# Performance work log

Hardware: AMD Instinct MI355X
Metric: run time of the kernel (lower is better)

## Reference

```python
import jax, jax.numpy as jnp
import numpy as np
from jax import lax

B, C, H, W = 2, 96, 64, 64
D_INNER, D_STATE, DT_RANK, K = 192, 16, 6, 4
EPS = 1e-5


def _ln(x, g, b):
    mu = jnp.mean(x, -1, keepdims=True)
    var = jnp.var(x, -1, keepdims=True)
    return (x - mu) * lax.rsqrt(var + EPS) * g + b


def setup_inputs() -> dict:
    key = jax.random.key(0)
    ks = jax.random.split(key, 10)
    f = lambda k, s, sc=0.02: jax.random.normal(k, s, dtype=jnp.float32) * sc
    return {
        "rgb": jax.random.normal(ks[0], (B, C, H, W), dtype=jnp.float32),
        "t": jax.random.normal(ks[1], (B, C, H, W), dtype=jnp.float32),
        "conv_w": f(ks[2], (C, 2 * C, 3, 3), 0.05),
        "conv_b": jnp.zeros((C,), jnp.float32),
        "bn_gamma": jnp.ones((C,), jnp.float32),
        "bn_beta": jnp.zeros((C,), jnp.float32),
        "bn_mean": jnp.zeros((C,), jnp.float32),
        "bn_var": jnp.ones((C,), jnp.float32),
        "ln_gamma": jnp.ones((C,), jnp.float32),
        "ln_beta": jnp.zeros((C,), jnp.float32),
        "in_proj_w": f(ks[3], (2 * D_INNER, C)),
        "dwconv_w": f(ks[4], (D_INNER, 1, 3, 3), 0.1),
        "dwconv_b": jnp.zeros((D_INNER,), jnp.float32),
        "x_proj_w": f(ks[5], (K, DT_RANK + 2 * D_STATE, D_INNER)),
        "dt_w": f(ks[6], (K, D_INNER, DT_RANK), 0.1),
        "dt_b": jnp.full((K, D_INNER), float(np.log(np.expm1(0.01))), jnp.float32),
        "A_logs": jnp.log(jnp.tile(jnp.arange(1, D_STATE + 1, dtype=jnp.float32), (K * D_INNER, 1))),
        "Ds": jnp.ones((K * D_INNER,), jnp.float32),
        "out_norm_gamma": jnp.ones((D_INNER,), jnp.float32),
        "out_norm_beta": jnp.zeros((D_INNER,), jnp.float32),
        "out_proj_w": f(ks[7], (C, D_INNER)),
    }


def _forward(rgb, t, conv_w, conv_b, bn_gamma, bn_beta, bn_mean, bn_var,
             ln_gamma, ln_beta, in_proj_w, dwconv_w, dwconv_b, x_proj_w,
             dt_w, dt_b, A_logs, Ds, out_norm_gamma, out_norm_beta, out_proj_w):
    dn = ("NCHW", "OIHW", "NCHW")
    # BasicConv: conv + BN(eval) + ReLU (dropout inactive in eval)
    x = jnp.concatenate([rgb, t], axis=1)
    x = lax.conv_general_dilated(x, conv_w, (1, 1), "SAME", dimension_numbers=dn)
    x = x + conv_b[None, :, None, None]
    x = (x - bn_mean[None, :, None, None]) * lax.rsqrt(bn_var[None, :, None, None] + EPS)
    x = x * bn_gamma[None, :, None, None] + bn_beta[None, :, None, None]
    x = jax.nn.relu(x)
    # permute to (B,H,W,C) and LayerNorm over channels
    x = _ln(jnp.transpose(x, (0, 2, 3, 1)), ln_gamma, ln_beta)
    # ---- SS2D ----
    xz = jnp.einsum("bhwc,ec->bhwe", x, in_proj_w)  # e = 2*d_inner
    xc, z = jnp.split(xz, 2, axis=-1)
    xc = jnp.transpose(xc, (0, 3, 1, 2))  # (B, d_inner, H, W)
    xc = lax.conv_general_dilated(xc, dwconv_w, (1, 1), "SAME",
                                  dimension_numbers=dn, feature_group_count=D_INNER)
    xc = jax.nn.silu(xc + dwconv_b[None, :, None, None])
    L = H * W
    # cross-scan: row-major, col-major, and their reverses -> (B,4,d,L)
    x_flat = xc.reshape(B, D_INNER, L)
    x_tr = jnp.transpose(xc, (0, 1, 3, 2)).reshape(B, D_INNER, L)
    xs = jnp.stack([x_flat, x_tr], axis=1)
    xs = jnp.concatenate([xs, xs[..., ::-1]], axis=1)  # (B,K,d,L)
    x_dbl = jnp.einsum("bkdl,kcd->bkcl", xs, x_proj_w)
    dts = x_dbl[:, :, :DT_RANK]
    Bs = x_dbl[:, :, DT_RANK:DT_RANK + D_STATE]  # (B,K,N,L)
    Cs = x_dbl[:, :, DT_RANK + D_STATE:]         # (B,K,N,L)
    dts = jnp.einsum("bkrl,kdr->bkdl", dts, dt_w)
    A = -jnp.exp(A_logs).reshape(K, D_INNER, D_STATE)
    Dsk = Ds.reshape(K, D_INNER)
    delta = jax.nn.softplus(dts + dt_b[None, :, :, None])  # (B,K,d,L)
    du = delta * xs

    def step(h, inp):
        dl, dul, Bl, Cl = inp  # (B,K,d),(B,K,d),(B,K,N),(B,K,N)
        h = h * jnp.exp(dl[..., None] * A) + dul[..., None] * Bl[:, :, None, :]
        y = jnp.einsum("bkdn,bkn->bkd", h, Cl)
        return h, y

    h0 = jnp.zeros((B, K, D_INNER, D_STATE), delta.dtype)
    _, ys = lax.scan(step, h0, (
        jnp.transpose(delta, (3, 0, 1, 2)),
        jnp.transpose(du, (3, 0, 1, 2)),
        jnp.transpose(Bs, (3, 0, 1, 2)),
        jnp.transpose(Cs, (3, 0, 1, 2)),
    ))
    out_y = jnp.transpose(ys, (1, 2, 3, 0)) + xs * Dsk[None, :, :, None]  # (B,K,d,L)
    # merge four scan directions back to row-major order
    inv_y = out_y[:, 2:4, :, ::-1]
    wh_y = jnp.transpose(out_y[:, 1].reshape(B, D_INNER, W, H), (0, 1, 3, 2)).reshape(B, D_INNER, L)
    invwh_y = jnp.transpose(inv_y[:, 1].reshape(B, D_INNER, W, H), (0, 1, 3, 2)).reshape(B, D_INNER, L)
    y = out_y[:, 0] + inv_y[:, 0] + wh_y + invwh_y  # (B,d,L)
    y = jnp.transpose(y, (0, 2, 1)).reshape(B, H, W, D_INNER)
    y = _ln(y, out_norm_gamma, out_norm_beta)
    y = y * jax.nn.silu(z)
    out = jnp.einsum("bhwd,cd->bhwc", y, out_proj_w)
    return jnp.transpose(out, (0, 3, 1, 2))  # (B,C,H,W)


def reference(rgb, t, conv_w, conv_b, bn_gamma, bn_beta, bn_mean, bn_var,
              ln_gamma, ln_beta, in_proj_w, dwconv_w, dwconv_b, x_proj_w,
              dt_w, dt_b, A_logs, Ds, out_norm_gamma, out_norm_beta, out_proj_w):
    return _forward(rgb, t, conv_w, conv_b, bn_gamma, bn_beta, bn_mean, bn_var,
                    ln_gamma, ln_beta, in_proj_w, dwconv_w, dwconv_b, x_proj_w,
                    dt_w, dt_b, A_logs, Ds, out_norm_gamma, out_norm_beta, out_proj_w)
```

## Files before the change

kernel.cpp:

```cpp
#include <hip/hip_runtime.h>
#include <math.h>

#define HW 4096
#define CC 96
#define DD 192
#define NS 16
#define KK 4
#define LC 64
#define NC 64
#define NCH (8*DD*NS)

__device__ __forceinline__ float siluf(float x){ return x / (1.f + __expf(-x)); }
__device__ __forceinline__ float softplus_fast(float x){ return (x > 20.f) ? x : __logf(1.f + __expf(x)); }

__device__ __forceinline__ int lmap_xs(int k, int l){
  if (k == 1) return ((l & 63) << 6) | (l >> 6);
  if (k == 2) return (HW - 1) - l;
  if (k == 3) { int r = (HW - 1) - l; return ((r & 63) << 6) | (r >> 6); }
  return l;
}

__global__ void k_prep(const float* __restrict__ cw, const float* __restrict__ xpw,
                       float* __restrict__ wT, float* __restrict__ xpwT){
  int o = blockIdx.x*256 + threadIdx.x;
  if (o < 165888){
    int co = o % 96; int rest = o / 96; int tap = rest % 9; int cig = rest / 9;
    wT[o] = cw[((size_t)co*192 + cig)*9 + tap];
  } else if (o < 165888 + 29184){
    int o2 = o - 165888;
    int c = o2 % 38; int rest = o2 / 38; int d = rest % 192; int k = rest / 192;
    xpwT[o2] = xpw[((size_t)(k*38 + c))*192 + d];
  }
}

__global__ void __launch_bounds__(256, 4)
k_conv1(const float* __restrict__ rgb, const float* __restrict__ tt,
        const float* __restrict__ wT, float* __restrict__ pbuf){
  __shared__ float in_lds[6][6][68];
  __shared__ __align__(16) float w_lds[6][9][64];
  int bi = blockIdx.x;
  int kc  = bi & 15;        int ci0 = kc*12;
  int cog = (bi >> 4) & 1;  int co0 = cog*48;
  int b   = (bi >> 5) & 1;
  int pt  = bi >> 6;        int h0 = pt*4;
  int tid = threadIdx.x;
  int pg = tid & 31;  int r = pg >> 3;  int w0 = (pg & 7)*8;
  int cg = tid >> 5;  int co_t = cg*6;

  float acc[6][8];
  #pragma unroll
  for (int c = 0; c < 6; ++c)
    #pragma unroll
    for (int p = 0; p < 8; ++p) acc[c][p] = 0.f;

  for (int s = 0; s < 2; ++s){
    if (s) __syncthreads();
    if (tid < 72){ int side = tid & 1; int rr = (tid % 12) >> 1; int ci = tid / 12;
                   in_lds[ci][rr][side ? 65 : 0] = 0.f; }
    for (int i = tid; i < 2304; i += 256){
      int ci = i / 384; int rem = i - ci*384; int rr = rem >> 6; int w = rem & 63;
      int grow = h0 - 1 + rr;
      int cig = ci0 + s*6 + ci;
      float v = 0.f;
      if (grow >= 0 && grow < 64){
        const float* src = (cig < CC) ? (rgb + (size_t)(b*CC+cig)*HW)
                                      : (tt  + (size_t)(b*CC+cig-CC)*HW);
        v = src[grow*64 + w];
      }
      in_lds[ci][rr][w+1] = v;
    }
    for (int i = tid; i < 2592; i += 256){
      int co = i % 48; int rest = i / 48; int tap = rest % 9; int ci = rest / 9;
      w_lds[ci][tap][(co/6)*8 + (co%6)] =
          wT[((size_t)(ci0 + s*6 + ci)*9 + tap)*96 + co0 + co];
    }
    __syncthreads();
    #pragma unroll
    for (int ci = 0; ci < 6; ++ci){
      float rowv[3][10];
      #pragma unroll
      for (int rr = 0; rr < 3; ++rr){
        const float* rp = &in_lds[ci][r+rr][w0];
        float4 a = *(const float4*)rp;
        float4 bb = *(const float4*)(rp+4);
        float2 cc = *(const float2*)(rp+8);
        rowv[rr][0]=a.x; rowv[rr][1]=a.y; rowv[rr][2]=a.z; rowv[rr][3]=a.w;
        rowv[rr][4]=bb.x; rowv[rr][5]=bb.y; rowv[rr][6]=bb.z; rowv[rr][7]=bb.w;
        rowv[rr][8]=cc.x; rowv[rr][9]=cc.y;
      }
      #pragma unroll
      for (int tap = 0; tap < 9; ++tap){
        int rt = tap/3, ct = tap - rt*3;
        float4 wa = *(const float4*)&w_lds[ci][tap][cg*8];
        float2 wb = *(const float2*)&w_lds[ci][tap][cg*8+4];
        float wv[6] = {wa.x, wa.y, wa.z, wa.w, wb.x, wb.y};
        #pragma unroll
        for (int p = 0; p < 8; ++p){
          float iv = rowv[rt][p + ct];
          #pragma unroll
          for (int c = 0; c < 6; ++c) acc[c][p] += wv[c]*iv;
        }
      }
    }
  }
  #pragma unroll
  for (int p = 0; p < 8; ++p){
    int pix = (h0 + r)*64 + w0 + p;
    float* o = pbuf + (((size_t)kc*2 + b)*HW + pix)*CC + co0 + co_t;
    float2 o0 = {acc[0][p], acc[1][p]};
    float2 o1 = {acc[2][p], acc[3][p]};
    float2 o2 = {acc[4][p], acc[5][p]};
    *(float2*)&o[0] = o0; *(float2*)&o[2] = o1; *(float2*)&o[4] = o2;
  }
}

__global__ void k_convred(const float* __restrict__ pbuf, const float* __restrict__ cb,
                          const float* __restrict__ bng, const float* __restrict__ bnb,
                          const float* __restrict__ bnm, const float* __restrict__ bnv,
                          const float* __restrict__ lng, const float* __restrict__ lnb,
                          float* __restrict__ xn){
  __shared__ float sm[4], sm2[4], smu[2], srs[2];
  int tid = threadIdx.x;
  int half = tid >> 7;
  int c = tid & 127;
  int pixg = blockIdx.x*2 + half;
  int b = pixg >> 12; int pix = pixg & (HW-1);
  float v = 0.f;
  if (c < CC){
    #pragma unroll
    for (int kc = 0; kc < 16; ++kc)
      v += pbuf[(((size_t)kc*2 + b)*HW + pix)*CC + c];
    v += cb[c];
    v = (v - bnm[c]) * rsqrtf(bnv[c] + 1e-5f);
    v = v * bng[c] + bnb[c];
    v = fmaxf(v, 0.f);
  }
  float s = v, s2 = v*v;
  #pragma unroll
  for (int off = 32; off; off >>= 1){ s += __shfl_down(s, off); s2 += __shfl_down(s2, off); }
  if ((tid & 63) == 0){ sm[tid>>6] = s; sm2[tid>>6] = s2; }
  __syncthreads();
  if (tid < 2){
    float ts = sm[2*tid] + sm[2*tid+1];
    float ts2 = sm2[2*tid] + sm2[2*tid+1];
    float mu = ts * (1.f/CC);
    float var = ts2 * (1.f/CC) - mu*mu;
    smu[tid] = mu; srs[tid] = rsqrtf(var + 1e-5f);
  }
  __syncthreads();
  if (c < CC)
    xn[(size_t)pixg*CC + c] = (v - smu[half])*srs[half]*lng[c] + lnb[c];
}

__global__ void k_inproj(const float* __restrict__ xn, const float* __restrict__ ipw,
                         float* __restrict__ xz){
  __shared__ float As[64][97];
  __shared__ __align__(16) float Bs[96][68];
  int p0 = blockIdx.x*64;
  int e0 = blockIdx.y*64;
  int tid = threadIdx.x;
  for (int idx = tid; idx < 64*96; idx += 256){
    int r = idx/96, c = idx - r*96;
    As[r][c] = xn[(size_t)(p0+r)*96 + c];
  }
  for (int idx = tid; idx < 96*64; idx += 256){
    int c = idx/64, e = idx - c*64;
    Bs[c][e] = ipw[(size_t)(e0+e)*96 + c];
  }
  __syncthreads();
  int tx = tid & 15, ty = tid >> 4;
  float acc[4][4] = {};
  for (int c = 0; c < 96; ++c){
    float a[4];
    #pragma unroll
    for (int i = 0; i < 4; ++i) a[i] = As[ty*4+i][c];
    float4 bb = *(const float4*)&Bs[c][tx*4];
    float bv[4] = {bb.x, bb.y, bb.z, bb.w};
    #pragma unroll
    for (int i = 0; i < 4; ++i)
      #pragma unroll
      for (int j = 0; j < 4; ++j) acc[i][j] += a[i]*bv[j];
  }
  for (int i = 0; i < 4; ++i){
    float4 o = {acc[i][0], acc[i][1], acc[i][2], acc[i][3]};
    *(float4*)&xz[(size_t)(p0+ty*4+i)*384 + e0 + tx*4] = o;
  }
}

__global__ void k_dwconv(const float* __restrict__ xz, const float* __restrict__ dww,
                         const float* __restrict__ dwb, float* __restrict__ xc){
  int gid = blockIdx.x*256 + threadIdx.x;
  int dq = gid % 48; int bp = gid / 48;
  int d = dq*4;
  int pix = bp & (HW-1); int b = bp >> 12;
  int h = pix >> 6, w = pix & 63;
  float4 acc = *(const float4*)&dwb[d];
  float wreg[4][9];
  #pragma unroll
  for (int j = 0; j < 4; ++j)
    #pragma unroll
    for (int t = 0; t < 9; ++t) wreg[j][t] = dww[(d+j)*9 + t];
  #pragma unroll
  for (int dh = -1; dh <= 1; ++dh){
    int hh = h + dh;
    if (hh < 0 || hh > 63) continue;
    #pragma unroll
    for (int dw2 = -1; dw2 <= 1; ++dw2){
      int ww = w + dw2;
      if (ww < 0 || ww > 63) continue;
      float4 v = *(const float4*)&xz[((size_t)b*HW + hh*64 + ww)*384 + d];
      int t = (dh+1)*3 + (dw2+1);
      acc.x += v.x*wreg[0][t];
      acc.y += v.y*wreg[1][t];
      acc.z += v.z*wreg[2][t];
      acc.w += v.w*wreg[3][t];
    }
  }
  float4 o = {siluf(acc.x), siluf(acc.y), siluf(acc.z), siluf(acc.w)};
  *(float4*)&xc[(size_t)bp*DD + d] = o;
}

__global__ void __launch_bounds__(320)
k_xdbl(const float* __restrict__ xc, const float* __restrict__ xpwT,
       const float* __restrict__ dtw, const float* __restrict__ dtb,
       float* __restrict__ Bsb, float* __restrict__ Csb, float* __restrict__ dlt){
  __shared__ float xs_t[48*20];
  __shared__ float w_t[48*80];
  __shared__ float dts_s[2][16][8];
  int blk = blockIdx.x;
  int lt = blk & 255; int p = (blk >> 8) & 1; int b = blk >> 9;
  int l0 = lt*16;
  int tid = threadIdx.x;
  int lg = tid & 15, cg = tid >> 4;
  int c0 = cg*4;
  int b4kA = b*4 + p, b4kB = b*4 + p + 2;
  int wc = tid % 76;
  int wg = tid / 76;
  int kkW = (wc < 38) ? p : (p + 2);
  int ccW = (wc < 38) ? wc : wc - 38;

  float acc[4] = {0.f, 0.f, 0.f, 0.f};
  for (int ch = 0; ch < 4; ++ch){
    int d0 = ch*48;
    if (ch) __syncthreads();
    if (tid < 192){
      int j = tid & 15; int dq = tid >> 4;
      int l = l0 + j;
      int lm = (p == 0) ? l : (((l & 63) << 6) | (l >> 6));
      float4 v = *(const float4*)&xc[((size_t)b*HW + lm)*DD + d0 + dq*4];
      xs_t[(dq*4+0)*20 + j] = v.x;
      xs_t[(dq*4+1)*20 + j] = v.y;
      xs_t[(dq*4+2)*20 + j] = v.z;
      xs_t[(dq*4+3)*20 + j] = v.w;
    }
    if (wg < 4){
      #pragma unroll
      for (int dd = wg; dd < 48; dd += 4)
        w_t[dd*80 + wc] = xpwT[((size_t)kkW*192 + d0 + dd)*38 + ccW];
    }
    __syncthreads();
    #pragma unroll 4
    for (int dd = 0; dd < 48; ++dd){
      float4 wv = *(const float4*)&w_t[dd*80 + c0];
      float xv = xs_t[dd*20 + lg];
      acc[0] += wv.x*xv;
      acc[1] += wv.y*xv;
      acc[2] += wv.z*xv;
      acc[3] += wv.w*xv;
    }
  }
  {
    int lf = l0 + lg;
    int lr = HW - 1 - lf;
    #pragma unroll
    for (int j = 0; j < 4; ++j){
      int c = c0 + j;
      float v = acc[j];
      if      (c <  6) dts_s[0][lg][c] = v;
      else if (c < 22) Bsb [((size_t)b4kA*HW + lf)*NS + (c-6)]   = v;
      else if (c < 38) Csb [((size_t)b4kA*HW + lf)*NS + (c-22)]  = v;
      else if (c < 44) dts_s[1][lg][c-38] = v;
      else if (c < 60) Bsb [((size_t)b4kB*HW + lr)*NS + (c-44)]  = v;
      else if (c < 76) Csb [((size_t)b4kB*HW + lr)*NS + (c-60)]  = v;
    }
  }
  __syncthreads();

  for (int o = tid; o < 6144; o += 320){
    int dir = (o >= 3072) ? 1 : 0;
    int oo = o - dir*3072;
    int lj = oo / 192;
    int d  = oo - lj*192;
    int k  = dir ? (p + 2) : p;
    int b4k = dir ? b4kB : b4kA;
    int lout = dir ? (HW - 1 - (l0 + lj)) : (l0 + lj);
    const float* t = dts_s[dir][lj];
    const float* wp = &dtw[(size_t)(k*DD + d)*6];
    float s = dtb[k*DD + d] + t[0]*wp[0] + t[1]*wp[1] + t[2]*wp[2]
                            + t[3]*wp[3] + t[4]*wp[4] + t[5]*wp[5];
    dlt[((size_t)b4k*HW + lout)*DD + d] = softplus_fast(s);
  }
}

__global__ void k_scan1(const float* __restrict__ dlt, const float* __restrict__ xc,
                        const float* __restrict__ Bsb, const float* __restrict__ Alog,
                        float* __restrict__ Ac, float* __restrict__ Bc){
  int tid = blockIdx.x*256 + threadIdx.x;
  int ng = tid & 3;
  int t2 = tid >> 2;
  int d = t2 % DD;
  int rest = t2 / DD;
  int chunk = rest & (NC-1);
  int b4k = rest >> 6;
  int k = b4k & 3, b = b4k >> 2;
  float4 Af = *(const float4*)&Alog[(size_t)(k*DD+d)*NS + ng*4];
  float Av[4] = {-__expf(Af.x), -__expf(Af.y), -__expf(Af.z), -__expf(Af.w)};
  float h[4] = {0.f,0.f,0.f,0.f};
  float ap[4] = {1.f,1.f,1.f,1.f};
  int l0 = chunk*LC;
  const float* dp  = dlt + ((size_t)b4k*HW + l0)*DD + d;
  const float4* Bp4 = (const float4*)(Bsb + ((size_t)b4k*HW + l0)*NS) + ng;
  const float* xcb = xc + (size_t)b*HW*DD + d;
  float dvc = dp[0];
  float xvc = xcb[(size_t)lmap_xs(k, l0)*DD];
  float4 Bvc = Bp4[0];
  #pragma unroll 4
  for (int i = 0; i < LC; ++i){
    float dvn = 0.f, xvn = 0.f; float4 Bvn = {0.f,0.f,0.f,0.f};
    if (i+1 < LC){
      dvn = dp[(size_t)(i+1)*DD];
      xvn = xcb[(size_t)lmap_xs(k, l0+i+1)*DD];
      Bvn = Bp4[(size_t)(i+1)*4];
    }
    float du = dvc*xvc;
    float a0 = __expf(dvc*Av[0]), a1 = __expf(dvc*Av[1]),
          a2 = __expf(dvc*Av[2]), a3 = __expf(dvc*Av[3]);
    h[0] = h[0]*a0 + du*Bvc.x; ap[0] *= a0;
    h[1] = h[1]*a1 + du*Bvc.y; ap[1] *= a1;
    h[2] = h[2]*a2 + du*Bvc.z; ap[2] *= a2;
    h[3] = h[3]*a3 + du*Bvc.w; ap[3] *= a3;
    dvc = dvn; xvc = xvn; Bvc = Bvn;
  }
  size_t base = (size_t)chunk*NCH + (size_t)(b4k*DD + d)*NS + ng*4;
  *(float4*)&Ac[base] = make_float4(ap[0],ap[1],ap[2],ap[3]);
  *(float4*)&Bc[base] = make_float4(h[0],h[1],h[2],h[3]);
}

__global__ void k_scan2(float* __restrict__ Ac, const float* __restrict__ Bc){
  int chain = blockIdx.x*256 + threadIdx.x;
  float h = 0.f;
  for (int c = 0; c < NC; ++c){
    size_t idx = (size_t)c*NCH + chain;
    float a = Ac[idx], bv = Bc[idx];
    Ac[idx] = h;
    h = a*h + bv;
  }
}

__global__ void k_scan3(const float* __restrict__ dlt, const float* __restrict__ xc,
                        const float* __restrict__ Bsb, const float* __restrict__ Csb,
                        const float* __restrict__ Alog, const float* __restrict__ hst,
                        float* __restrict__ ys){
  int tid = blockIdx.x*256 + threadIdx.x;
  int ng = tid & 3;
  int t2 = tid >> 2;
  int d = t2 % DD;
  int rest = t2 / DD;
  int chunk = rest & (NC-1);
  int b4k = rest >> 6;
  int k = b4k & 3, b = b4k >> 2;
  float4 Af = *(const float4*)&Alog[(size_t)(k*DD+d)*NS + ng*4];
  float Av[4] = {-__expf(Af.x), -__expf(Af.y), -__expf(Af.z), -__expf(Af.w)};
  size_t hbase = (size_t)chunk*NCH + (size_t)(b4k*DD + d)*NS + ng*4;
  float4 hf = *(const float4*)&hst[hbase];
  float h[4] = {hf.x, hf.y, hf.z, hf.w};
  int l0 = chunk*LC;
  const float* dp  = dlt + ((size_t)b4k*HW + l0)*DD + d;
  const float4* Bp4 = (const float4*)(Bsb + ((size_t)b4k*HW + l0)*NS) + ng;
  const float4* Cp4 = (const float4*)(Csb + ((size_t)b4k*HW + l0)*NS) + ng;
  const float* xcb = xc + (size_t)b*HW*DD + d;
  float* yp = ys + ((size_t)b4k*HW + l0)*DD + d;
  float dvc = dp[0];
  float xvc = xcb[(size_t)lmap_xs(k, l0)*DD];
  float4 Bvc = Bp4[0];
  float4 Cvc = Cp4[0];
  #pragma unroll 4
  for (int i = 0; i < LC; ++i){
    float dvn = 0.f, xvn = 0.f; float4 Bvn = {0.f,0.f,0.f,0.f}, Cvn = {0.f,0.f,0.f,0.f};
    if (i+1 < LC){
      dvn = dp[(size_t)(i+1)*DD];
      xvn = xcb[(size_t)lmap_xs(k, l0+i+1)*DD];
      Bvn = Bp4[(size_t)(i+1)*4];
      Cvn = Cp4[(size_t)(i+1)*4];
    }
    float du = dvc*xvc;
    float a0 = __expf(dvc*Av[0]), a1 = __expf(dvc*Av[1]),
          a2 = __expf(dvc*Av[2]), a3 = __expf(dvc*Av[3]);
    h[0] = h[0]*a0 + du*Bvc.x;
    h[1] = h[1]*a1 + du*Bvc.y;
    h[2] = h[2]*a2 + du*Bvc.z;
    h[3] = h[3]*a3 + du*Bvc.w;
    float y = h[0]*Cvc.x + h[1]*Cvc.y + h[2]*Cvc.z + h[3]*Cvc.w;
    y += __shfl_xor(y, 1, 4);
    y += __shfl_xor(y, 2, 4);
    if (ng == 0) yp[(size_t)i*DD] = y;
    dvc = dvn; xvc = xvn; Bvc = Bvn; Cvc = Cvn;
  }
}

__global__ void k_gate(const float* __restrict__ ys, const float* __restrict__ xc,
                       const float* __restrict__ Ds, const float* __restrict__ xz,
                       const float* __restrict__ ong, const float* __restrict__ onb,
                       float* __restrict__ yg){
  int gt = blockIdx.x*256 + threadIdx.x;
  int wave = gt >> 6;
  int lane = gt & 63;
  int b = wave >> 12; int l = wave & (HW-1);
  int l1 = ((l & 63) << 6) | (l >> 6);
  size_t base = (size_t)b*KK*HW*DD;
  float v[3]; float s = 0.f, s2 = 0.f;
  #pragma unroll
  for (int j = 0; j < 3; ++j){
    int d = lane + j*64;
    float t;
    t  = ys[base + ((size_t)0*HW + l        )*DD + d];
    t += ys[base + ((size_t)1*HW + l1       )*DD + d];
    t += ys[base + ((size_t)2*HW + (HW-1-l ))*DD + d];
    t += ys[base + ((size_t)3*HW + (HW-1-l1))*DD + d];
    t += xc[((size_t)b*HW + l)*DD + d] * (Ds[d] + Ds[DD+d] + Ds[2*DD+d] + Ds[3*DD+d]);
    v[j] = t; s += t; s2 += t*t;
  }
  #pragma unroll
  for (int off = 32; off; off >>= 1){ s += __shfl_xor(s, off); s2 += __shfl_xor(s2, off); }
  float mu = s*(1.f/DD);
  float rstd = rsqrtf(s2*(1.f/DD) - mu*mu + 1e-5f);
  #pragma unroll
  for (int j = 0; j < 3; ++j){
    int d = lane + j*64;
    float z = xz[((size_t)b*HW + l)*384 + DD + d];
    float x = (v[j]-mu)*rstd*ong[d] + onb[d];
    yg[(size_t)wave*DD + d] = x * siluf(z);
  }
}

__global__ void k_outproj(const float* __restrict__ yg, const float* __restrict__ opw,
                          float* __restrict__ out){
  __shared__ float yl[48][36];
  __shared__ float wl[48][97];
  int blk = blockIdx.x;
  int b = blk >> 7; int pt = blk & 127;
  int px0 = pt*32;
  int tid = threadIdx.x;
  int pxg = tid & 7;
  int cgi = tid >> 3;
  float acc[4][3] = {};
  for (int k0 = 0; k0 < DD; k0 += 48){
    if (k0) __syncthreads();
    for (int i = tid; i < 32*48; i += 256){
      int r = i/48, k = i - r*48;
      yl[k][r] = yg[((size_t)b*HW + px0 + r)*DD + k0 + k];
    }
    for (int i = tid; i < 96*48; i += 256){
      int c = i/48, k = i - c*48;
      wl[k][c] = opw[(size_t)c*DD + k0 + k];
    }
    __syncthreads();
    #pragma unroll 4
    for (int k = 0; k < 48; ++k){
      float4 yv = *(const float4*)&yl[k][pxg*4];
      float w0 = wl[k][cgi*3], w1 = wl[k][cgi*3+1], w2 = wl[k][cgi*3+2];
      acc[0][0] += yv.x*w0; acc[0][1] += yv.x*w1; acc[0][2] += yv.x*w2;
      acc[1][0] += yv.y*w0; acc[1][1] += yv.y*w1; acc[1][2] += yv.y*w2;
      acc[2][0] += yv.z*w0; acc[2][1] += yv.z*w1; acc[2][2] += yv.z*w2;
      acc[3][0] += yv.w*w0; acc[3][1] += yv.w*w1; acc[3][2] += yv.w*w2;
    }
  }
  #pragma unroll
  for (int j = 0; j < 3; ++j){
    int c = cgi*3 + j;
    float4 o = {acc[0][j], acc[1][j], acc[2][j], acc[3][j]};
    *(float4*)&out[((size_t)b*CC + c)*HW + px0 + pxg*4] = o;
  }
}

extern "C" void kernel_launch(void* const* d_in, const int* in_sizes, int n_in,
                              void* d_out, int out_size, void* d_ws, size_t ws_size,
                              hipStream_t stream) {
  const float* rgb   = (const float*)d_in[0];
  const float* tt    = (const float*)d_in[1];
  const float* cw    = (const float*)d_in[2];
  const float* cb    = (const float*)d_in[3];
  const float* bng   = (const float*)d_in[4];
  const float* bnb   = (const float*)d_in[5];
  const float* bnm   = (const float*)d_in[6];
  const float* bnv   = (const float*)d_in[7];
  const float* lng   = (const float*)d_in[8];
  const float* lnb   = (const float*)d_in[9];
  const float* ipw   = (const float*)d_in[10];
  const float* dww   = (const float*)d_in[11];
  const float* dwb   = (const float*)d_in[12];
  const float* xpw   = (const float*)d_in[13];
  const float* dtw   = (const float*)d_in[14];
  const float* dtb   = (const float*)d_in[15];
  const float* Alog  = (const float*)d_in[16];
  const float* Ds    = (const float*)d_in[17];
  const float* ong   = (const float*)d_in[18];
  const float* onb   = (const float*)d_in[19];
  const float* opw   = (const float*)d_in[20];
  float* out = (float*)d_out;

  float* ws = (float*)d_ws;
  float* xn   = ws + 786432;
  float* xz   = ws + 1572864;
  float* xc   = ws + 4718592;
  float* Bsb  = ws + 6291456;
  float* Csb  = ws + 6815744;
  float* dlt  = ws + 7340032;
  float* ysb  = ws + 13631488;
  float* pbuf = ws + 1572864;
  float* Ac   = ws;
  float* Bc   = ysb;
  float* yg   = ws + 7340032;
  float* wT   = ws + 16777216;
  float* xpwT = ws + 16943104;

  k_prep<<<762, 256, 0, stream>>>(cw, xpw, wT, xpwT);
  k_conv1<<<1024, 256, 0, stream>>>(rgb, tt, wT, pbuf);
  k_convred<<<4096, 256, 0, stream>>>(pbuf, cb, bng, bnb, bnm, bnv, lng, lnb, xn);
  dim3 g2(128, 6);
  k_inproj<<<g2, 256, 0, stream>>>(xn, ipw, xz);
  k_dwconv<<<1536, 256, 0, stream>>>(xz, dww, dwb, xc);
  k_xdbl<<<1024, 320, 0, stream>>>(xc, xpwT, dtw, dtb, Bsb, Csb, dlt);
  k_scan1<<<1536, 256, 0, stream>>>(dlt, xc, Bsb, Alog, Ac, Bc);
  k_scan2<<<96, 256, 0, stream>>>(Ac, Bc);
  k_scan3<<<1536, 256, 0, stream>>>(dlt, xc, Bsb, Csb, Alog, Ac, ysb);
  k_gate<<<2048, 256, 0, stream>>>(ysb, xc, Ds, xz, ong, onb, yg);
  k_outproj<<<256, 256, 0, stream>>>(yg, opw, out);
}
```

Baseline: 233.2 us.

## Halve conv split-K partitions and spread scan states over eight lanes per channel

The conv kernel now splits the 192 input channels into 8 partitions of 24 instead of 16 of 12, each block looping over four LDS stages. This halves the partial-sum buffer that the reduction kernel reads. The chunked scan kernels now give each thread 2 SSM states instead of 4, with 8 lanes per channel, doubling the thread count for more parallelism and shorter per-thread serial work. The cost is fewer conv blocks, an extra shuffle step in scan3, and more redundant per-step loads of delta and x.

```diff
diff --git a/kernel.cpp b/kernel.cpp
--- a/kernel.cpp
+++ b/kernel.cpp
@@ -39,10 +39,10 @@
   __shared__ float in_lds[6][6][68];
   __shared__ __align__(16) float w_lds[6][9][64];
   int bi = blockIdx.x;
-  int kc  = bi & 15;        int ci0 = kc*12;
-  int cog = (bi >> 4) & 1;  int co0 = cog*48;
-  int b   = (bi >> 5) & 1;
-  int pt  = bi >> 6;        int h0 = pt*4;
+  int kc  = bi & 7;         int ci0 = kc*24;
+  int cog = (bi >> 3) & 1;  int co0 = cog*48;
+  int b   = (bi >> 4) & 1;
+  int pt  = bi >> 5;        int h0 = pt*4;
   int tid = threadIdx.x;
   int pg = tid & 31;  int r = pg >> 3;  int w0 = (pg & 7)*8;
   int cg = tid >> 5;  int co_t = cg*6;
@@ -53,7 +53,7 @@
     #pragma unroll
     for (int p = 0; p < 8; ++p) acc[c][p] = 0.f;
 
-  for (int s = 0; s < 2; ++s){
+  for (int s = 0; s < 4; ++s){
     if (s) __syncthreads();
     if (tid < 72){ int side = tid & 1; int rr = (tid % 12) >> 1; int ci = tid / 12;
                    in_lds[ci][rr][side ? 65 : 0] = 0.f; }
@@ -128,7 +128,7 @@
   float v = 0.f;
   if (c < CC){
     #pragma unroll
-    for (int kc = 0; kc < 16; ++kc)
+    for (int kc = 0; kc < 8; ++kc)
       v += pbuf[(((size_t)kc*2 + b)*HW + pix)*CC + c];
     v += cb[c];
     v = (v - bnm[c]) * rsqrtf(bnv[c] + 1e-5f);
@@ -306,44 +306,40 @@
                         const float* __restrict__ Bsb, const float* __restrict__ Alog,
                         float* __restrict__ Ac, float* __restrict__ Bc){
   int tid = blockIdx.x*256 + threadIdx.x;
-  int ng = tid & 3;
-  int t2 = tid >> 2;
+  int ng = tid & 7;
+  int t2 = tid >> 3;
   int d = t2 % DD;
   int rest = t2 / DD;
   int chunk = rest & (NC-1);
   int b4k = rest >> 6;
   int k = b4k & 3, b = b4k >> 2;
-  float4 Af = *(const float4*)&Alog[(size_t)(k*DD+d)*NS + ng*4];
-  float Av[4] = {-__expf(Af.x), -__expf(Af.y), -__expf(Af.z), -__expf(Af.w)};
-  float h[4] = {0.f,0.f,0.f,0.f};
-  float ap[4] = {1.f,1.f,1.f,1.f};
+  float2 Af = *(const float2*)&Alog[(size_t)(k*DD+d)*NS + ng*2];
+  float Av0 = -__expf(Af.x), Av1 = -__expf(Af.y);
+  float h0 = 0.f, h1 = 0.f, ap0 = 1.f, ap1 = 1.f;
   int l0 = chunk*LC;
   const float* dp  = dlt + ((size_t)b4k*HW + l0)*DD + d;
-  const float4* Bp4 = (const float4*)(Bsb + ((size_t)b4k*HW + l0)*NS) + ng;
+  const float2* Bp2 = (const float2*)(Bsb + ((size_t)b4k*HW + l0)*NS) + ng;
   const float* xcb = xc + (size_t)b*HW*DD + d;
   float dvc = dp[0];
   float xvc = xcb[(size_t)lmap_xs(k, l0)*DD];
-  float4 Bvc = Bp4[0];
+  float2 Bvc = Bp2[0];
   #pragma unroll 4
   for (int i = 0; i < LC; ++i){
-    float dvn = 0.f, xvn = 0.f; float4 Bvn = {0.f,0.f,0.f,0.f};
+    float dvn = 0.f, xvn = 0.f; float2 Bvn = {0.f,0.f};
     if (i+1 < LC){
       dvn = dp[(size_t)(i+1)*DD];
       xvn = xcb[(size_t)lmap_xs(k, l0+i+1)*DD];
-      Bvn = Bp4[(size_t)(i+1)*4];
+      Bvn = Bp2[(size_t)(i+1)*8];
     }
     float du = dvc*xvc;
-    float a0 = __expf(dvc*Av[0]), a1 = __expf(dvc*Av[1]),
-          a2 = __expf(dvc*Av[2]), a3 = __expf(dvc*Av[3]);
-    h[0] = h[0]*a0 + du*Bvc.x; ap[0] *= a0;
-    h[1] = h[1]*a1 + du*Bvc.y; ap[1] *= a1;
-    h[2] = h[2]*a2 + du*Bvc.z; ap[2] *= a2;
-    h[3] = h[3]*a3 + du*Bvc.w; ap[3] *= a3;
+    float a0 = __expf(dvc*Av0), a1 = __expf(dvc*Av1);
+    h0 = h0*a0 + du*Bvc.x; ap0 *= a0;
+    h1 = h1*a1 + du*Bvc.y; ap1 *= a1;
     dvc = dvn; xvc = xvn; Bvc = Bvn;
   }
-  size_t base = (size_t)chunk*NCH + (size_t)(b4k*DD + d)*NS + ng*4;
-  *(float4*)&Ac[base] = make_float4(ap[0],ap[1],ap[2],ap[3]);
-  *(float4*)&Bc[base] = make_float4(h[0],h[1],h[2],h[3]);
+  size_t base = (size_t)chunk*NCH + (size_t)(b4k*DD + d)*NS + ng*2;
+  *(float2*)&Ac[base] = make_float2(ap0, ap1);
+  *(float2*)&Bc[base] = make_float2(h0, h1);
 }
 
 __global__ void k_scan2(float* __restrict__ Ac, const float* __restrict__ Bc){
@@ -362,47 +358,45 @@
                         const float* __restrict__ Alog, const float* __restrict__ hst,
                         float* __restrict__ ys){
   int tid = blockIdx.x*256 + threadIdx.x;
-  int ng = tid & 3;
-  int t2 = tid >> 2;
+  int ng = tid & 7;
+  int t2 = tid >> 3;
   int d = t2 % DD;
   int rest = t2 / DD;
   int chunk = rest & (NC-1);
   int b4k = rest >> 6;
   int k = b4k & 3, b = b4k >> 2;
-  float4 Af = *(const float4*)&Alog[(size_t)(k*DD+d)*NS + ng*4];
-  float Av[4] = {-__expf(Af.x), -__expf(Af.y), -__expf(Af.z), -__expf(Af.w)};
-  size_t hbase = (size_t)chunk*NCH + (size_t)(b4k*DD + d)*NS + ng*4;
-  float4 hf = *(const float4*)&hst[hbase];
-  float h[4] = {hf.x, hf.y, hf.z, hf.w};
+  float2 Af = *(const float2*)&Alog[(size_t)(k*DD+d)*NS + ng*2];
+  float Av0 = -__expf(Af.x), Av1 = -__expf(Af.y);
+  size_t hbase = (size_t)chunk*NCH + (size_t)(b4k*DD + d)*NS + ng*2;
+  float2 hf = *(const float2*)&hst[hbase];
+  float h0 = hf.x, h1 = hf.y;
   int l0 = chunk*LC;
   const float* dp  = dlt + ((size_t)b4k*HW + l0)*DD + d;
-  const float4* Bp4 = (const float4*)(Bsb + ((size_t)b4k*HW + l0)*NS) + ng;
-  const float4* Cp4 = (const float4*)(Csb + ((size_t)b4k*HW + l0)*NS) + ng;
+  const float2* Bp2 = (const float2*)(Bsb + ((size_t)b4k*HW + l0)*NS) + ng;
+  const float2* Cp2 = (const float2*)(Csb + ((size_t)b4k*HW + l0)*NS) + ng;
   const float* xcb = xc + (size_t)b*HW*DD + d;
   float* yp = ys + ((size_t)b4k*HW + l0)*DD + d;
   float dvc = dp[0];
   float xvc = xcb[(size_t)lmap_xs(k, l0)*DD];
-  float4 Bvc = Bp4[0];
-  float4 Cvc = Cp4[0];
+  float2 Bvc = Bp2[0];
+  float2 Cvc = Cp2[0];
   #pragma unroll 4
   for (int i = 0; i < LC; ++i){
-    float dvn = 0.f, xvn = 0.f; float4 Bvn = {0.f,0.f,0.f,0.f}, Cvn = {0.f,0.f,0.f,0.f};
+    float dvn = 0.f, xvn = 0.f; float2 Bvn = {0.f,0.f}, Cvn = {0.f,0.f};
     if (i+1 < LC){
       dvn = dp[(size_t)(i+1)*DD];
       xvn = xcb[(size_t)lmap_xs(k, l0+i+1)*DD];
-      Bvn = Bp4[(size_t)(i+1)*4];
-      Cvn = Cp4[(size_t)(i+1)*4];
+      Bvn = Bp2[(size_t)(i+1)*8];
+      Cvn = Cp2[(size_t)(i+1)*8];
     }
     float du = dvc*xvc;
-    float a0 = __expf(dvc*Av[0]), a1 = __expf(dvc*Av[1]),
-          a2 = __expf(dvc*Av[2]), a3 = __expf(dvc*Av[3]);
-    h[0] = h[0]*a0 + du*Bvc.x;
-    h[1] = h[1]*a1 + du*Bvc.y;
-    h[2] = h[2]*a2 + du*Bvc.z;
-    h[3] = h[3]*a3 + du*Bvc.w;
-    float y = h[0]*Cvc.x + h[1]*Cvc.y + h[2]*Cvc.z + h[3]*Cvc.w;
-    y += __shfl_xor(y, 1, 4);
-    y += __shfl_xor(y, 2, 4);
+    float a0 = __expf(dvc*Av0), a1 = __expf(dvc*Av1);
+    h0 = h0*a0 + du*Bvc.x;
+    h1 = h1*a1 + du*Bvc.y;
+    float y = h0*Cvc.x + h1*Cvc.y;
+    y += __shfl_xor(y, 1, 8);
+    y += __shfl_xor(y, 2, 8);
+    y += __shfl_xor(y, 4, 8);
     if (ng == 0) yp[(size_t)i*DD] = y;
     dvc = dvn; xvc = xvn; Bvc = Bvn; Cvc = Cvn;
   }
@@ -525,15 +519,15 @@
   float* xpwT = ws + 16943104;
 
   k_prep<<<762, 256, 0, stream>>>(cw, xpw, wT, xpwT);
-  k_conv1<<<1024, 256, 0, stream>>>(rgb, tt, wT, pbuf);
+  k_conv1<<<512, 256, 0, stream>>>(rgb, tt, wT, pbuf);
   k_convred<<<4096, 256, 0, stream>>>(pbuf, cb, bng, bnb, bnm, bnv, lng, lnb, xn);
   dim3 g2(128, 6);
   k_inproj<<<g2, 256, 0, stream>>>(xn, ipw, xz);
   k_dwconv<<<1536, 256, 0, stream>>>(xz, dww, dwb, xc);
   k_xdbl<<<1024, 320, 0, stream>>>(xc, xpwT, dtw, dtb, Bsb, Csb, dlt);
-  k_scan1<<<1536, 256, 0, stream>>>(dlt, xc, Bsb, Alog, Ac, Bc);
+  k_scan1<<<3072, 256, 0, stream>>>(dlt, xc, Bsb, Alog, Ac, Bc);
   k_scan2<<<96, 256, 0, stream>>>(Ac, Bc);
-  k_scan3<<<1536, 256, 0, stream>>>(dlt, xc, Bsb, Csb, Alog, Ac, ysb);
+  k_scan3<<<3072, 256, 0, stream>>>(dlt, xc, Bsb, Csb, Alog, Ac, ysb);
   k_gate<<<2048, 256, 0, stream>>>(ysb, xc, Ds, xz, ong, onb, yg);
   k_outproj<<<256, 256, 0, stream>>>(yg, opw, out);
 }
```

New measurement: 287.1 us. 23.1% more time.
